# Optimization experiments

Hardware: AMD Instinct MI355X
Metric: run time of the kernel (lower is better)

Reference implementation:

```python
import jax, jax.numpy as jnp
import numpy as np

KH = KW = 3          # kernel_size
PAD = 1              # padding (stride = 1)
K = KH * KW          # 9 kernel taps


def _bilinear_sample(x, ys, xs):
    """Bilinear sample with zero padding outside the image.
    x: [C,H,W]; ys, xs: [K,H,W] float sample coords. Returns [C,K,H,W]."""
    C, H, W = x.shape
    y0f = jnp.floor(ys)
    x0f = jnp.floor(xs)
    wy1 = ys - y0f
    wx1 = xs - x0f
    wy0 = 1.0 - wy1
    wx0 = 1.0 - wx1
    y0 = y0f.astype(jnp.int32)
    x0 = x0f.astype(jnp.int32)
    y1 = y0 + 1
    x1 = x0 + 1
    xf = x.reshape(C, H * W)

    def gather(yi, xi, wgt):
        valid = (yi >= 0) & (yi < H) & (xi >= 0) & (xi < W)
        idx = jnp.clip(yi, 0, H - 1) * W + jnp.clip(xi, 0, W - 1)  # [K,H,W]
        v = xf[:, idx.reshape(-1)].reshape(C, K, H, W)
        return v * (wgt * valid)[None]

    return (gather(y0, x0, wy0 * wx0) + gather(y0, x1, wy0 * wx1)
            + gather(y1, x0, wy1 * wx0) + gather(y1, x1, wy1 * wx1))


def _deform_conv2d(x, off, w):
    """DCNv1 for one (batch, group) slice.
    x: [C,H,W]; off: [2K,H,W] mmcv layout (dy,dx per tap); w: [Cout,Cin,KH,KW]."""
    C, H, W = x.shape
    off = off.reshape(K, 2, H, W)
    dy, dx = off[:, 0], off[:, 1]                       # [K,H,W]
    ky = (jnp.arange(K) // KW).astype(x.dtype)
    kx = (jnp.arange(K) % KW).astype(x.dtype)
    hh = jnp.arange(H, dtype=x.dtype)
    ww = jnp.arange(W, dtype=x.dtype)
    ys = dy + ky[:, None, None] - PAD + hh[None, :, None]   # stride=1
    xs = dx + kx[:, None, None] - PAD + ww[None, None, :]
    sampled = _bilinear_sample(x, ys, xs)               # [C,K,H,W]
    return jnp.einsum('ikhw,oik->ohw', sampled, w.reshape(w.shape[0], w.shape[1], K))


def reference(feat, offset, weight):
    """feat: [B,C,T,H,W]; offset: [B,2K,T,H,W]; weight: [T,Cout,Cin,KH,KW].
    groups=T, deform_groups=T -> each temporal slice is an independent DCN."""
    ft = jnp.transpose(feat, (0, 2, 1, 3, 4))    # [B,T,C,H,W]
    ot = jnp.transpose(offset, (0, 2, 1, 3, 4))  # [B,T,2K,H,W]
    per_t = jax.vmap(_deform_conv2d, in_axes=(0, 0, 0))       # over T (weight per-T)
    per_b = jax.vmap(per_t, in_axes=(0, 0, None))             # over B (weight shared)
    out = per_b(ft, ot, weight)                  # [B,T,C,H,W]
    return jnp.transpose(out, (0, 2, 1, 3, 4))   # [B,C,T,H,W]


def setup_inputs() -> dict:
    key = jax.random.key(0)
    k1, k2, k3 = jax.random.split(key, 3)
    B, C, T, H, W = 2, 32, 8, 192, 192
    feat = jax.random.normal(k1, (B, C, T, H, W), dtype=jnp.float32)
    offset = jax.random.normal(k2, (B, 2 * K, T, H, W), dtype=jnp.float32)
    weight = jax.random.normal(k3, (T, C, C, KH, KW), dtype=jnp.float32) * 0.05
    return {"feat": feat, "offset": offset, "weight": weight}
```

## Files before the change

kernel.cpp:

```cpp
#include <hip/hip_runtime.h>
#include <hip/hip_bf16.h>


#define CIN   32
#define COUT  32
#define TT    8
#define HH    192
#define WW    192
#define KK    9
#define HWSZ  (HH * WW)
#define PLANE (TT * HWSZ)

#define TILE_W 32
#define TILE_H 8
#define HALO   4
#define HROWS  (TILE_H + 2 * HALO + 1)
#define HCOLS  (TILE_W + 2 * HALO + 1)
#define HPLANE (HROWS * HCOLS)
#define HPLANE_B (HPLANE * 16)
#define HROW_B  (HCOLS * 16)

typedef __attribute__((ext_vector_type(8))) short short8;
typedef __attribute__((ext_vector_type(4))) float f32x4;

union U4S8 { uint4 u; short8 s; };

__device__ __forceinline__ float bl_lo(uint u) { return __uint_as_float(u << 16); }
__device__ __forceinline__ float bl_hi(uint u) { return __uint_as_float(u & 0xffff0000u); }

__device__ __forceinline__ uint pk_bf16(float lo, float hi) {
    float2 p; p.x = lo; p.y = hi;
    __hip_bfloat162 b = __float22bfloat162_rn(p);
    union { __hip_bfloat162 b; uint u; } cv; cv.b = b;
    return cv.u;
}

__device__ __forceinline__ uint blerp_pack(uint a, uint b, uint c, uint d,
                                           float w00, float w01, float w10, float w11) {
    float lo = w00 * bl_lo(a) + w01 * bl_lo(b) + w10 * bl_lo(c) + w11 * bl_lo(d);
    float hi = w00 * bl_hi(a) + w01 * bl_hi(b) + w10 * bl_hi(c) + w11 * bl_hi(d);
    return pk_bf16(lo, hi);
}

__global__ __launch_bounds__(256) void transpose_bf16_kernel(
    const float* __restrict__ feat, uint* __restrict__ tf)
{
    __shared__ float tile[CIN][257];
    const int p0 = blockIdx.x * 256;
    const int t  = blockIdx.y;
    const int b  = blockIdx.z;

    const float* src = feat + (size_t)b * CIN * PLANE + (size_t)t * HWSZ + p0;
    #pragma unroll
    for (int c = 0; c < CIN; ++c)
        tile[c][threadIdx.x] = src[(size_t)c * PLANE + threadIdx.x];
    __syncthreads();

    uint* dst = tf + ((size_t)(b * TT + t) * HWSZ + p0) * (CIN / 2);
    #pragma unroll
    for (int it = 0; it < 16; ++it) {
        int i  = it * 256 + threadIdx.x;
        int p  = i >> 4, c2 = i & 15;
        dst[p * 16 + c2] = pk_bf16(tile[2 * c2][p], tile[2 * c2 + 1][p]);
    }
}

__global__ __launch_bounds__(256) void wprep_kernel(
    const float* __restrict__ wt, ushort* __restrict__ wfrag)
{
    int idx = blockIdx.x * 256 + threadIdx.x;
    if (idx >= TT * KK * 2 * 64 * 8) return;
    int t  = idx / (KK * 1024);
    int f  = idx % (KK * 1024);
    int k  = f >> 10;
    int r2 = f & 1023;
    int n    = r2 >> 9;
    int lane = (r2 >> 3) & 63;
    int j    = r2 & 7;
    int o = n * 16 + (lane & 15);
    int c = (lane >> 4) * 8 + j;
    float v = wt[(((size_t)t * COUT + o) * CIN + c) * KK + k];
    __hip_bfloat16 hb = __float2bfloat16(v);
    union { __hip_bfloat16 b; ushort u; } cv; cv.b = hb;
    wfrag[idx] = cv.u;
}

__global__ __launch_bounds__(256, 3) void dcn_mfma_kernel(
    const uint* __restrict__ tf,
    const float* __restrict__ offset,
    const ushort* __restrict__ wfrag,
    float* __restrict__ out)
{
    __shared__ uint4 halo4[4 * HPLANE];
    __shared__ f32x4 wts[256];
    __shared__ uint2 meta2[256];

    const int tid  = threadIdx.x;
    const int lane = tid & 63;
    const int wv   = tid >> 6;
    const int lane15 = lane & 15;
    const int quad   = lane >> 4;

    const int w0 = blockIdx.x * TILE_W;
    const int h0 = blockIdx.y * TILE_H;
    const int bt = blockIdx.z;
    const int t  = bt & (TT - 1);
    const int b  = bt >> 3;

    const int hlo = h0 - HALO, wlo = w0 - HALO;
    const int hhi = hlo + (HROWS - 1), whi = wlo + (HCOLS - 1);

    const uint4* tfs4 = (const uint4*)tf + (size_t)bt * HWSZ * 4;

    #pragma unroll
    for (int it = 0; it < 11; ++it) {
        int idx = it * 256 + tid;
        if (idx < 4 * HPLANE) {
            int r    = idx / (HCOLS * 4);
            int rem  = idx - r * (HCOLS * 4);
            int pv   = rem >> 2;
            int part = rem & 3;
            int gy = min(max(hlo + r, 0), HH - 1);
            int gx = min(max(wlo + pv, 0), WW - 1);
            halo4[part * HPLANE + r * HCOLS + pv] = tfs4[(gy * WW + gx) * 4 + part];
        }
    }

    const int prow = h0 + 2 * wv + (lane >> 5);
    const int pcol = w0 + (lane & 31);
    const int px_own = (2 * wv + (lane >> 5)) * 32 + (lane & 31);
    const float* offp = offset + (size_t)b * 2 * KK * PLANE + (size_t)t * HWSZ
                      + prow * WW + pcol;

    const uint4* wfp = (const uint4*)(wfrag + (size_t)t * KK * 2 * 64 * 8);

    f32x4 acc[4][2];
    #pragma unroll
    for (int i = 0; i < 4; ++i)
        #pragma unroll
        for (int n = 0; n < 2; ++n) {
            acc[i][n][0] = 0.f; acc[i][n][1] = 0.f;
            acc[i][n][2] = 0.f; acc[i][n][3] = 0.f;
        }

    int pxc[4];
    #pragma unroll
    for (int i = 0; i < 4; ++i)
        pxc[i] = (2 * wv + (i >> 1)) * 32 + ((i & 1) << 4) + lane15;

    const uint qb = (uint)quad * HPLANE_B;
    const char* hbase = (const char*)halo4;

    __syncthreads();

    float dy = offp[0];
    float dx = offp[(size_t)PLANE];

    #pragma unroll
    for (int k = 0; k < KK; ++k) {
        const int ky = k / 3 - 1;
        const int kx = k % 3 - 1;

        float dyn = 0.f, dxn = 0.f;
        if (k < KK - 1) {
            dyn = offp[(size_t)(2 * k + 2) * PLANE];
            dxn = offp[(size_t)(2 * k + 3) * PLANE];
        }

        U4S8 bf0, bf1;
        bf0.u = wfp[(k * 2 + 0) * 64 + lane];
        bf1.u = wfp[(k * 2 + 1) * 64 + lane];

        {
            const float ys = (float)(prow + ky) + dy;
            const float xs = (float)(pcol + kx) + dx;
            const float y0f = floorf(ys), x0f = floorf(xs);
            const float wy1 = ys - y0f,  wx1 = xs - x0f;
            const float wy0 = 1.f - wy1, wx0 = 1.f - wx1;

            const int y0 = (int)y0f, x0i = (int)x0f;
            const int y1 = y0 + 1,   x1 = x0i + 1;

            const float vy0 = (y0 >= 0 && y0 < HH) ? 1.f : 0.f;
            const float vy1 = (y1 >= 0 && y1 < HH) ? 1.f : 0.f;
            const float vx0 = (x0i >= 0 && x0i < WW) ? 1.f : 0.f;
            const float vx1 = (x1 >= 0 && x1 < WW) ? 1.f : 0.f;

            const int cy0 = min(max(y0, 0), HH - 1);
            const int cy1 = min(max(y1, 0), HH - 1);
            const int cx0 = min(max(x0i, 0), WW - 1);
            const int cx1 = min(max(x1, 0), WW - 1);

            f32x4 w4;
            w4[0] = wy0 * wx0 * vy0 * vx0;
            w4[1] = wy0 * wx1 * vy0 * vx1;
            w4[2] = wy1 * wx0 * vy1 * vx0;
            w4[3] = wy1 * wx1 * vy1 * vx1;

            const bool inH = (cy0 >= hlo) & (cy1 <= hhi) & (cx0 >= wlo) & (cx1 <= whi);
            uint mx;
            if (inH) {
                const int a00 = ((cy0 - hlo) * HCOLS + (cx0 - wlo)) * 16;
                const int dcb = (cx1 - cx0) << 4;
                const int drb = (cy1 - cy0) * HROW_B;
                mx = (uint)a00 | ((uint)dcb << 14) | ((uint)drb << 19);
            } else {
                mx = 0x80000000u;
            }
            const uint my = (uint)cy0 | ((uint)cx0 << 8)
                          | ((uint)cy1 << 16) | ((uint)cx1 << 24);

            wts[px_own]   = w4;
            meta2[px_own] = make_uint2(mx, my);
        }

        #pragma unroll
        for (int i = 0; i < 4; ++i) {
            const f32x4 w4  = wts[pxc[i]];
            const uint2 mm  = meta2[pxc[i]];

            uint4 q00, q01, q10, q11;
            if ((int)mm.x >= 0) {
                const uint a00 = (mm.x & 0x3fffu) + qb;
                const uint dc  = (mm.x >> 14) & 0x1fu;
                const uint dr  = (mm.x >> 19);
                q00 = *(const uint4*)(hbase + a00);
                q01 = *(const uint4*)(hbase + (a00 + dc));
                q10 = *(const uint4*)(hbase + (a00 + dr));
                q11 = *(const uint4*)(hbase + (a00 + dc + dr));
            } else {
                const int cy0 = mm.y & 255,         cx0 = (mm.y >> 8) & 255;
                const int cy1 = (mm.y >> 16) & 255, cx1 = mm.y >> 24;
                q00 = tfs4[(cy0 * WW + cx0) * 4 + quad];
                q01 = tfs4[(cy0 * WW + cx1) * 4 + quad];
                q10 = tfs4[(cy1 * WW + cx0) * 4 + quad];
                q11 = tfs4[(cy1 * WW + cx1) * 4 + quad];
            }

            U4S8 af;
            af.u.x = blerp_pack(q00.x, q01.x, q10.x, q11.x, w4[0], w4[1], w4[2], w4[3]);
            af.u.y = blerp_pack(q00.y, q01.y, q10.y, q11.y, w4[0], w4[1], w4[2], w4[3]);
            af.u.z = blerp_pack(q00.z, q01.z, q10.z, q11.z, w4[0], w4[1], w4[2], w4[3]);
            af.u.w = blerp_pack(q00.w, q01.w, q10.w, q11.w, w4[0], w4[1], w4[2], w4[3]);

            acc[i][0] = __builtin_amdgcn_mfma_f32_16x16x32_bf16(af.s, bf0.s, acc[i][0], 0, 0, 0);
            acc[i][1] = __builtin_amdgcn_mfma_f32_16x16x32_bf16(af.s, bf1.s, acc[i][1], 0, 0, 0);
        }

        dy = dyn; dx = dxn;
    }

    float* ob = out + (size_t)b * COUT * PLANE + (size_t)t * HWSZ;
    #pragma unroll
    for (int i = 0; i < 4; ++i) {
        const int hp    = h0 + 2 * wv + (i >> 1);
        const int wbase = w0 + ((i & 1) << 4) + quad * 4;
        #pragma unroll
        for (int n = 0; n < 2; ++n) {
            const int o = n * 16 + lane15;
            float* op = ob + (size_t)o * PLANE + hp * WW + wbase;
            #pragma unroll
            for (int r = 0; r < 4; ++r) op[r] = acc[i][n][r];
        }
    }
}

__global__ __launch_bounds__(256) void dcn_fp32_kernel(
    const float* __restrict__ feat,
    const float* __restrict__ offset,
    const float* __restrict__ weight,
    float* __restrict__ out)
{
    __shared__ float sw[KK * CIN * COUT];
    const int tid = threadIdx.x;
    const int t   = blockIdx.y;
    const int b   = blockIdx.z;
    {
        const float* wg = weight + (size_t)t * (COUT * CIN * KK);
        #pragma unroll
        for (int j = 0; j < (KK * CIN * COUT) / 256; ++j) {
            int i  = tid + j * 256;
            int k  = i % KK;
            int oc = i / KK;
            sw[(k * CIN + (oc % CIN)) * COUT + (oc / CIN)] = wg[i];
        }
    }
    __syncthreads();

    const int pix = blockIdx.x * 256 + tid;
    const int h   = pix / WW;
    const int w   = pix % WW;

    float acc[COUT];
    #pragma unroll
    for (int o = 0; o < COUT; ++o) acc[o] = 0.0f;

    const float* offp = offset + ((size_t)(b * 2 * KK) * TT + t) * HWSZ + pix;
    float offv[2 * KK];
    #pragma unroll
    for (int j = 0; j < 2 * KK; ++j) offv[j] = offp[(size_t)j * PLANE];

    const float* fbase = feat + ((size_t)(b * CIN) * TT + t) * HWSZ;

    for (int k = 0; k < KK; ++k) {
        const float ys = (float)(h + k / 3 - 1) + offv[2 * k];
        const float xs = (float)(w + k % 3 - 1) + offv[2 * k + 1];
        const float y0f = floorf(ys), x0f = floorf(xs);
        const float wy1 = ys - y0f, wx1 = xs - x0f;
        const float wy0 = 1.0f - wy1, wx0 = 1.0f - wx1;
        const int y0 = (int)y0f, x0 = (int)x0f, y1 = y0 + 1, x1 = x0 + 1;
        const bool vy0 = (y0 >= 0) && (y0 < HH), vy1 = (y1 >= 0) && (y1 < HH);
        const bool vx0 = (x0 >= 0) && (x0 < WW), vx1 = (x1 >= 0) && (x1 < WW);
        const int cy0 = min(max(y0, 0), HH - 1), cy1 = min(max(y1, 0), HH - 1);
        const int cx0 = min(max(x0, 0), WW - 1), cx1 = min(max(x1, 0), WW - 1);
        const float w00 = wy0 * wx0 * ((vy0 && vx0) ? 1.0f : 0.0f);
        const float w01 = wy0 * wx1 * ((vy0 && vx1) ? 1.0f : 0.0f);
        const float w10 = wy1 * wx0 * ((vy1 && vx0) ? 1.0f : 0.0f);
        const float w11 = wy1 * wx1 * ((vy1 && vx1) ? 1.0f : 0.0f);
        const int i00 = cy0 * WW + cx0, i01 = cy0 * WW + cx1;
        const int i10 = cy1 * WW + cx0, i11 = cy1 * WW + cx1;

        const float*  sp   = fbase;
        const float4* wrow = (const float4*)&sw[k * CIN * COUT];
        for (int c = 0; c < CIN; ++c) {
            const float v = w00 * sp[i00] + w01 * sp[i01]
                          + w10 * sp[i10] + w11 * sp[i11];
            const float4* wp = wrow + c * (COUT / 4);
            #pragma unroll
            for (int o4 = 0; o4 < COUT / 4; ++o4) {
                const float4 wv = wp[o4];
                acc[4 * o4 + 0] += v * wv.x;
                acc[4 * o4 + 1] += v * wv.y;
                acc[4 * o4 + 2] += v * wv.z;
                acc[4 * o4 + 3] += v * wv.w;
            }
            sp += PLANE;
        }
    }

    float* op = out + ((size_t)(b * COUT) * TT + t) * HWSZ + pix;
    #pragma unroll
    for (int o = 0; o < COUT; ++o) op[(size_t)o * PLANE] = acc[o];
}

extern "C" void kernel_launch(void* const* d_in, const int* in_sizes, int n_in,
                              void* d_out, int out_size, void* d_ws, size_t ws_size,
                              hipStream_t stream) {
    const float* feat   = (const float*)d_in[0];
    const float* offset = (const float*)d_in[1];
    const float* weight = (const float*)d_in[2];
    float* out = (float*)d_out;

    const size_t tf_bytes = (size_t)2 * TT * HWSZ * CIN * sizeof(ushort);
    const size_t wf_bytes = (size_t)TT * KK * 2 * 64 * 8 * sizeof(ushort);

    if (ws_size >= tf_bytes + wf_bytes) {
        uint*   tf    = (uint*)d_ws;
        ushort* wfrag = (ushort*)((char*)d_ws + tf_bytes);

        transpose_bf16_kernel<<<dim3(HWSZ / 256, TT, 2), dim3(256), 0, stream>>>(feat, tf);
        wprep_kernel<<<dim3((TT * KK * 2 * 64 * 8 + 255) / 256), dim3(256), 0, stream>>>(weight, wfrag);
        dcn_mfma_kernel<<<dim3(WW / TILE_W, HH / TILE_H, 2 * TT), dim3(256), 0, stream>>>(
            tf, offset, wfrag, out);
    } else {
        dcn_fp32_kernel<<<dim3(HWSZ / 256, TT, 2), dim3(256), 0, stream>>>(feat, offset, weight, out);
    }
}
```

Before: 248.2 us.

## Prefetch all offsets upfront, pack metadata into one word, use packed-float bilinear math

All 18 offset values per pixel are now loaded into registers before the halo fill, so their global latency overlaps the shared-memory staging instead of being prefetched one tap ahead. Per-pixel metadata shrinks from two words to one by encoding the out-of-halo fallback coordinates as a base plus 1-bit deltas, which halves those LDS writes and reads. The bilinear interpolation is rewritten on float2 vectors so the compiler can emit packed FMA instructions, and the high bf16 half skips its mask. The trade-off is more registers held for the offsets, which may pressure occupancy at 3 waves per SIMD, and a slight change in rounding because the high half is no longer masked.

```diff
diff --git a/kernel.cpp b/kernel.cpp
--- a/kernel.cpp
+++ b/kernel.cpp
@@ -22,11 +22,9 @@
 
 typedef __attribute__((ext_vector_type(8))) short short8;
 typedef __attribute__((ext_vector_type(4))) float f32x4;
+typedef __attribute__((ext_vector_type(2))) float f32x2;
 
 union U4S8 { uint4 u; short8 s; };
-
-__device__ __forceinline__ float bl_lo(uint u) { return __uint_as_float(u << 16); }
-__device__ __forceinline__ float bl_hi(uint u) { return __uint_as_float(u & 0xffff0000u); }
 
 __device__ __forceinline__ uint pk_bf16(float lo, float hi) {
     float2 p; p.x = lo; p.y = hi;
@@ -35,11 +33,20 @@
     return cv.u;
 }
 
-__device__ __forceinline__ uint blerp_pack(uint a, uint b, uint c, uint d,
-                                           float w00, float w01, float w10, float w11) {
-    float lo = w00 * bl_lo(a) + w01 * bl_lo(b) + w10 * bl_lo(c) + w11 * bl_lo(d);
-    float hi = w00 * bl_hi(a) + w01 * bl_hi(b) + w10 * bl_hi(c) + w11 * bl_hi(d);
-    return pk_bf16(lo, hi);
+__device__ __forceinline__ f32x2 up2(uint u) {
+    f32x2 r;
+    r.x = __uint_as_float(u << 16);
+    r.y = __uint_as_float(u);
+    return r;
+}
+
+__device__ __forceinline__ uint blerp4(uint a, uint b, uint c, uint d,
+                                       f32x2 s00, f32x2 s01, f32x2 s10, f32x2 s11) {
+    f32x2 r = up2(a) * s00;
+    r = up2(b) * s01 + r;
+    r = up2(c) * s10 + r;
+    r = up2(d) * s11 + r;
+    return pk_bf16(r.x, r.y);
 }
 
 __global__ __launch_bounds__(256) void transpose_bf16_kernel(
@@ -93,7 +100,7 @@
 {
     __shared__ uint4 halo4[4 * HPLANE];
     __shared__ f32x4 wts[256];
-    __shared__ uint2 meta2[256];
+    __shared__ uint  meta1[256];
 
     const int tid  = threadIdx.x;
     const int lane = tid & 63;
@@ -111,6 +118,16 @@
     const int hhi = hlo + (HROWS - 1), whi = wlo + (HCOLS - 1);
 
     const uint4* tfs4 = (const uint4*)tf + (size_t)bt * HWSZ * 4;
+
+    const int prow = h0 + 2 * wv + (lane >> 5);
+    const int pcol = w0 + (lane & 31);
+    const int px_own = (2 * wv + (lane >> 5)) * 32 + (lane & 31);
+    const float* offp = offset + (size_t)b * 2 * KK * PLANE + (size_t)t * HWSZ
+                      + prow * WW + pcol;
+
+    float offv[2 * KK];
+    #pragma unroll
+    for (int j = 0; j < 2 * KK; ++j) offv[j] = offp[(size_t)j * PLANE];
 
     #pragma unroll
     for (int it = 0; it < 11; ++it) {
@@ -126,12 +143,6 @@
         }
     }
 
-    const int prow = h0 + 2 * wv + (lane >> 5);
-    const int pcol = w0 + (lane & 31);
-    const int px_own = (2 * wv + (lane >> 5)) * 32 + (lane & 31);
-    const float* offp = offset + (size_t)b * 2 * KK * PLANE + (size_t)t * HWSZ
-                      + prow * WW + pcol;
-
     const uint4* wfp = (const uint4*)(wfrag + (size_t)t * KK * 2 * 64 * 8);
 
     f32x4 acc[4][2];
@@ -153,25 +164,18 @@
 
     __syncthreads();
 
-    float dy = offp[0];
-    float dx = offp[(size_t)PLANE];
-
     #pragma unroll
     for (int k = 0; k < KK; ++k) {
         const int ky = k / 3 - 1;
         const int kx = k % 3 - 1;
 
-        float dyn = 0.f, dxn = 0.f;
-        if (k < KK - 1) {
-            dyn = offp[(size_t)(2 * k + 2) * PLANE];
-            dxn = offp[(size_t)(2 * k + 3) * PLANE];
-        }
-
         U4S8 bf0, bf1;
         bf0.u = wfp[(k * 2 + 0) * 64 + lane];
         bf1.u = wfp[(k * 2 + 1) * 64 + lane];
 
         {
+            const float dy = offv[2 * k];
+            const float dx = offv[2 * k + 1];
             const float ys = (float)(prow + ky) + dy;
             const float xs = (float)(pcol + kx) + dx;
             const float y0f = floorf(ys), x0f = floorf(xs);
@@ -192,10 +196,12 @@
             const int cx1 = min(max(x1, 0), WW - 1);
 
             f32x4 w4;
-            w4[0] = wy0 * wx0 * vy0 * vx0;
-            w4[1] = wy0 * wx1 * vy0 * vx1;
-            w4[2] = wy1 * wx0 * vy1 * vx0;
-            w4[3] = wy1 * wx1 * vy1 * vx1;
+            const float wy0v = wy0 * vy0, wy1v = wy1 * vy1;
+            const float wx0v = wx0 * vx0, wx1v = wx1 * vx1;
+            w4[0] = wy0v * wx0v;
+            w4[1] = wy0v * wx1v;
+            w4[2] = wy1v * wx0v;
+            w4[3] = wy1v * wx1v;
 
             const bool inH = (cy0 >= hlo) & (cy1 <= hhi) & (cx0 >= wlo) & (cx1 <= whi);
             uint mx;
@@ -205,32 +211,36 @@
                 const int drb = (cy1 - cy0) * HROW_B;
                 mx = (uint)a00 | ((uint)dcb << 14) | ((uint)drb << 19);
             } else {
-                mx = 0x80000000u;
+                mx = 0x80000000u | (uint)cy0 | ((uint)cx0 << 8)
+                   | ((uint)(cy1 - cy0) << 16) | ((uint)(cx1 - cx0) << 17);
             }
-            const uint my = (uint)cy0 | ((uint)cx0 << 8)
-                          | ((uint)cy1 << 16) | ((uint)cx1 << 24);
 
             wts[px_own]   = w4;
-            meta2[px_own] = make_uint2(mx, my);
+            meta1[px_own] = mx;
         }
 
         #pragma unroll
         for (int i = 0; i < 4; ++i) {
-            const f32x4 w4  = wts[pxc[i]];
-            const uint2 mm  = meta2[pxc[i]];
+            const f32x4 w4 = wts[pxc[i]];
+            const uint  mm = meta1[pxc[i]];
+            f32x2 s00; s00.x = w4[0]; s00.y = w4[0];
+            f32x2 s01; s01.x = w4[1]; s01.y = w4[1];
+            f32x2 s10; s10.x = w4[2]; s10.y = w4[2];
+            f32x2 s11; s11.x = w4[3]; s11.y = w4[3];
 
             uint4 q00, q01, q10, q11;
-            if ((int)mm.x >= 0) {
-                const uint a00 = (mm.x & 0x3fffu) + qb;
-                const uint dc  = (mm.x >> 14) & 0x1fu;
-                const uint dr  = (mm.x >> 19);
+            if ((int)mm >= 0) {
+                const uint a00 = (mm & 0x3fffu) + qb;
+                const uint dc  = (mm >> 14) & 0x1fu;
+                const uint dr  = mm >> 19;
                 q00 = *(const uint4*)(hbase + a00);
                 q01 = *(const uint4*)(hbase + (a00 + dc));
                 q10 = *(const uint4*)(hbase + (a00 + dr));
                 q11 = *(const uint4*)(hbase + (a00 + dc + dr));
             } else {
-                const int cy0 = mm.y & 255,         cx0 = (mm.y >> 8) & 255;
-                const int cy1 = (mm.y >> 16) & 255, cx1 = mm.y >> 24;
+                const int cy0 = mm & 255,        cx0 = (mm >> 8) & 255;
+                const int cy1 = cy0 + ((mm >> 16) & 1);
+                const int cx1 = cx0 + ((mm >> 17) & 1);
                 q00 = tfs4[(cy0 * WW + cx0) * 4 + quad];
                 q01 = tfs4[(cy0 * WW + cx1) * 4 + quad];
                 q10 = tfs4[(cy1 * WW + cx0) * 4 + quad];
@@ -238,16 +248,14 @@
             }
 
             U4S8 af;
-            af.u.x = blerp_pack(q00.x, q01.x, q10.x, q11.x, w4[0], w4[1], w4[2], w4[3]);
-            af.u.y = blerp_pack(q00.y, q01.y, q10.y, q11.y, w4[0], w4[1], w4[2], w4[3]);
-            af.u.z = blerp_pack(q00.z, q01.z, q10.z, q11.z, w4[0], w4[1], w4[2], w4[3]);
-            af.u.w = blerp_pack(q00.w, q01.w, q10.w, q11.w, w4[0], w4[1], w4[2], w4[3]);
+            af.u.x = blerp4(q00.x, q01.x, q10.x, q11.x, s00, s01, s10, s11);
+            af.u.y = blerp4(q00.y, q01.y, q10.y, q11.y, s00, s01, s10, s11);
+            af.u.z = blerp4(q00.z, q01.z, q10.z, q11.z, s00, s01, s10, s11);
+            af.u.w = blerp4(q00.w, q01.w, q10.w, q11.w, s00, s01, s10, s11);
 
             acc[i][0] = __builtin_amdgcn_mfma_f32_16x16x32_bf16(af.s, bf0.s, acc[i][0], 0, 0, 0);
             acc[i][1] = __builtin_amdgcn_mfma_f32_16x16x32_bf16(af.s, bf1.s, acc[i][1], 0, 0, 0);
         }
-
-        dy = dyn; dx = dxn;
     }
 
     float* ob = out + (size_t)b * COUT * PLANE + (size_t)t * HWSZ;
```

Measured after the change: 239.9 us. 1.03x faster.
